# Optimization experiments

Measured on AMD Instinct MI355X. Metric: run time of the kernel, lower is better.

The kernel has to match this reference:

```python
import jax, jax.numpy as jnp
import numpy as np

B, D = 512, 1024
NK, DIMS = 160, 3  # hardcoded in the layer: Dense(160*3), reshape (-1,160,3)


def setup_inputs() -> dict:
    key = jax.random.key(0)
    k1, k2 = jax.random.split(key)
    inputs = jax.random.normal(k1, (B, D), dtype=jnp.float32)
    W = jax.random.normal(k2, (D, NK * DIMS), dtype=jnp.float32) * 0.02
    b = jnp.zeros((NK * DIMS,), dtype=jnp.float32)
    return {"inputs": inputs, "W": W, "b": b}


def reference(inputs, W, b):
    # dense projection: [B, D] @ [D, 480] -> [B, 480]
    x = inputs @ W + b
    act = x.reshape(-1, NK, DIMS)                       # [B, 160, 3]
    # pairwise diffs: [B, 160, 3, 1] - [1, 160, 3, B] -> [B, 160, 3, B]
    diffs = act[:, :, :, None] - jnp.transpose(act, (1, 2, 0))[None]
    abs_diffs = jnp.sum(jnp.abs(diffs), axis=2)         # [B, 160, B]
    minibatch_features = jnp.sum(jnp.exp(-abs_diffs), axis=2)  # [B, 160]
    return jnp.concatenate([inputs, minibatch_features], axis=1)  # [B, D+160]
```

## Files before the change

### kernel.cpp

```cpp
#include <hip/hip_runtime.h>
#include <hip/hip_bf16.h>

#define B_SZ 512
#define D_SZ 1024
#define NK 160
#define NCOL 480
#define OUTW 1184
#define LOG2E 1.44269504088896340736f

typedef __attribute__((ext_vector_type(8))) short bf16x8;
typedef __attribute__((ext_vector_type(4))) float f32x4;

__device__ __forceinline__ unsigned int f32_bf16_rne(float f) {
    unsigned int u = __float_as_uint(f);
    u += 0x7fffu + ((u >> 16) & 1u);
    return u >> 16;
}
__device__ __forceinline__ unsigned int pk2(float x, float y) {
    return f32_bf16_rne(x) | (f32_bf16_rne(y) << 16);
}
__device__ __forceinline__ float bf16u_to_f32(unsigned int h) {
    return __uint_as_float(h << 16);
}

__global__ __launch_bounds__(256) void mbd_gemm_kernel(
    const float* __restrict__ A,
    const float* __restrict__ W,
    const float* __restrict__ bias,
    float* __restrict__ out,
    float* __restrict__ act_t)
{
    __shared__ char lds[32768];
    const int bid = blockIdx.x;
    const int t = threadIdx.x;

    {
        const float4 v = *reinterpret_cast<const float4*>(&A[bid * D_SZ + t * 4]);
        *reinterpret_cast<float4*>(&out[bid * OUTW + t * 4]) = v;
    }
    if (bid >= 480) return;

    const int g = bid >> 3;
    const int bm = (bid & 7) * 2 + (g & 1);
    const int bn = g >> 1;
    const int i0 = bm * 32, c0 = bn * 16;
    const int w = __builtin_amdgcn_readfirstlane(t >> 6);
    const int l = t & 63, lhi = l >> 4, llo = l & 15;

    const int arow = t >> 3, aseg = t & 7;
    const int wcol = t & 15, wkb = t >> 4;
    const int aswz = (arow & 7) << 4;
    const int wswz = (wcol & 7) << 4;
    const float* __restrict__ aptr = A + (size_t)(i0 + arow) * D_SZ + aseg * 16;
    const float* __restrict__ wptr = W + (size_t)wkb * 8 * NCOL + (c0 + wcol);

    f32x4 acc = {0.f, 0.f, 0.f, 0.f};
    float4 ra[4];
    float rw[8];

    auto issue_loads = [&](int k0) {
#pragma unroll
        for (int s = 0; s < 4; ++s)
            ra[s] = *reinterpret_cast<const float4*>(aptr + k0 + s * 4);
#pragma unroll
        for (int j = 0; j < 8; ++j)
            rw[j] = wptr[(size_t)(k0 + j) * NCOL];
    };
    auto write_stage = [&](int buf) {
        char* base = lds + buf * 16384;
        uint4 p0, p1;
        p0.x = pk2(ra[0].x, ra[0].y); p0.y = pk2(ra[0].z, ra[0].w);
        p0.z = pk2(ra[1].x, ra[1].y); p0.w = pk2(ra[1].z, ra[1].w);
        p1.x = pk2(ra[2].x, ra[2].y); p1.y = pk2(ra[2].z, ra[2].w);
        p1.z = pk2(ra[3].x, ra[3].y); p1.w = pk2(ra[3].z, ra[3].w);
        char* arp = base + arow * 256;
        *reinterpret_cast<uint4*>(arp + ((aseg * 32) ^ aswz)) = p0;
        *reinterpret_cast<uint4*>(arp + ((aseg * 32 + 16) ^ aswz)) = p1;
        unsigned int h[8]; float lo[8];
#pragma unroll
        for (int j = 0; j < 8; ++j) {
            h[j] = f32_bf16_rne(rw[j]);
            lo[j] = rw[j] - bf16u_to_f32(h[j]);
        }
        uint4 ph, pl;
        ph.x = h[0] | (h[1] << 16); ph.y = h[2] | (h[3] << 16);
        ph.z = h[4] | (h[5] << 16); ph.w = h[6] | (h[7] << 16);
        pl.x = pk2(lo[0], lo[1]); pl.y = pk2(lo[2], lo[3]);
        pl.z = pk2(lo[4], lo[5]); pl.w = pk2(lo[6], lo[7]);
        const int wo = (wkb * 16) ^ wswz;
        *reinterpret_cast<uint4*>(base + 8192 + wcol * 256 + wo) = ph;
        *reinterpret_cast<uint4*>(base + 12288 + wcol * 256 + wo) = pl;
    };
    auto compute = [&](int buf) {
        const char* base = lds + buf * 16384;
        const char* bsrc = base + ((w >= 2) ? 12288 : 8192);
        const int wrow = (w & 1) * 16;
#pragma unroll
        for (int ks = 0; ks < 4; ++ks) {
            const int koff = (lhi * 16 + ks * 64) ^ ((llo & 7) << 4);
            const bf16x8 af = *reinterpret_cast<const bf16x8*>(base + (wrow + llo) * 256 + koff);
            const bf16x8 bf = *reinterpret_cast<const bf16x8*>(bsrc + llo * 256 + koff);
            acc = __builtin_amdgcn_mfma_f32_16x16x32_bf16(af, bf, acc, 0, 0, 0);
        }
    };

    issue_loads(0);
    write_stage(0);
    __syncthreads();
    for (int ch = 0; ch < 8; ++ch) {
        if (ch < 7) issue_loads((ch + 1) * 128);
        compute(ch & 1);
        if (ch < 7) {
            __syncthreads();
            write_stage((ch + 1) & 1);
            __syncthreads();
        }
    }
    __syncthreads();
    float4* comb = reinterpret_cast<float4*>(lds);
    if (w >= 2) comb[(w - 2) * 64 + l] = make_float4(acc[0], acc[1], acc[2], acc[3]);
    __syncthreads();
    if (w < 2) {
        const float4 lo4 = comb[w * 64 + l];
        const int col = c0 + llo;
        const float bs = bias[col];
        float4 o;
        o.x = (acc[0] + lo4.x + bs) * LOG2E;
        o.y = (acc[1] + lo4.y + bs) * LOG2E;
        o.z = (acc[2] + lo4.z + bs) * LOG2E;
        o.w = (acc[3] + lo4.w + bs) * LOG2E;
        *reinterpret_cast<float4*>(&act_t[(size_t)col * B_SZ + i0 + (w & 1) * 16 + lhi * 4]) = o;
    }
}

__global__ __launch_bounds__(64) void mbd_pairwise_kernel(
    const float* __restrict__ act_t,
    float* __restrict__ out)
{
    __shared__ float4 as4[B_SZ];
    const int bid = blockIdx.x;
    const int klin = (bid & 7) * 320 + (bid >> 3);
    const int k = klin >> 4;
    const int c = klin & 15;
    const int t = threadIdx.x;

    const float* __restrict__ p0 = act_t + (size_t)(3 * k + 0) * B_SZ;
    const float* __restrict__ p1 = act_t + (size_t)(3 * k + 1) * B_SZ;
    const float* __restrict__ p2 = act_t + (size_t)(3 * k + 2) * B_SZ;
#pragma unroll
    for (int s = 0; s < 8; ++s) {
        const int idx = t + s * 64;
        as4[idx] = make_float4(p0[idx], p1[idx], p2[idx], 0.f);
    }
    __syncthreads();

    const int jq = t >> 3;
    const int rg = t & 7;
    const int r0 = c * 32 + rg * 4;
    const float4 a0 = as4[r0 + 0];
    const float4 a1 = as4[r0 + 1];
    const float4 a2 = as4[r0 + 2];
    const float4 a3 = as4[r0 + 3];

    float acc0 = 0.f, acc1 = 0.f, acc2 = 0.f, acc3 = 0.f;
#pragma unroll 8
    for (int jj = 0; jj < 64; ++jj) {
        const float4 av = as4[jq + jj * 8];
        acc0 += __builtin_amdgcn_exp2f(-(fabsf(a0.x - av.x) + fabsf(a0.y - av.y) + fabsf(a0.z - av.z)));
        acc1 += __builtin_amdgcn_exp2f(-(fabsf(a1.x - av.x) + fabsf(a1.y - av.y) + fabsf(a1.z - av.z)));
        acc2 += __builtin_amdgcn_exp2f(-(fabsf(a2.x - av.x) + fabsf(a2.y - av.y) + fabsf(a2.z - av.z)));
        acc3 += __builtin_amdgcn_exp2f(-(fabsf(a3.x - av.x) + fabsf(a3.y - av.y) + fabsf(a3.z - av.z)));
    }
#pragma unroll
    for (int m = 8; m <= 32; m <<= 1) {
        acc0 += __shfl_xor(acc0, m);
        acc1 += __shfl_xor(acc1, m);
        acc2 += __shfl_xor(acc2, m);
        acc3 += __shfl_xor(acc3, m);
    }
    if (t < 8) {
        out[(size_t)(r0 + 0) * OUTW + D_SZ + k] = acc0;
        out[(size_t)(r0 + 1) * OUTW + D_SZ + k] = acc1;
        out[(size_t)(r0 + 2) * OUTW + D_SZ + k] = acc2;
        out[(size_t)(r0 + 3) * OUTW + D_SZ + k] = acc3;
    }
}

extern "C" void kernel_launch(void* const* d_in, const int* in_sizes, int n_in,
                              void* d_out, int out_size, void* d_ws, size_t ws_size,
                              hipStream_t stream)
{
    const float* inputs = (const float*)d_in[0];
    const float* W      = (const float*)d_in[1];
    const float* bias   = (const float*)d_in[2];
    float* out = (float*)d_out;
    float* act_t = (float*)d_ws;

    mbd_gemm_kernel<<<512, 256, 0, stream>>>(inputs, W, bias, out, act_t);
    mbd_pairwise_kernel<<<NK * 16, 64, 0, stream>>>(act_t, out);
}
```

Measured before the change: 26.97 us.

## Pre-split W into transposed bf16 hi/lo buffers and use an LDS-free split-K GEMM

```diff
diff --git a/kernel.cpp b/kernel.cpp
--- a/kernel.cpp
+++ b/kernel.cpp
@@ -23,113 +23,94 @@
     return __uint_as_float(h << 16);
 }
 
+__global__ __launch_bounds__(256) void mbd_prep_kernel(
+    const float* __restrict__ A,
+    const float* __restrict__ W,
+    unsigned int* __restrict__ Whi_u,
+    unsigned int* __restrict__ Wlo_u,
+    float* __restrict__ out)
+{
+    __shared__ float lds_t[64][33];
+    const int b = blockIdx.x, t = threadIdx.x;
+    if (b < 512) {
+        const float4 v = *reinterpret_cast<const float4*>(&A[b * D_SZ + t * 4]);
+        *reinterpret_cast<float4*>(&out[b * OUTW + t * 4]) = v;
+        return;
+    }
+    const int bw = b - 512;
+    const int c0 = (bw % 15) * 32;
+    const int k0 = (bw / 15) * 64;
+#pragma unroll
+    for (int p = 0; p < 8; ++p) {
+        const int k = p * 8 + (t >> 5);
+        lds_t[k][t & 31] = W[(k0 + k) * NCOL + c0 + (t & 31)];
+    }
+    __syncthreads();
+#pragma unroll
+    for (int p = 0; p < 4; ++p) {
+        const int flat = p * 256 + t;
+        const int col = flat >> 5;
+        const int kkp = flat & 31;
+        const float w0 = lds_t[2 * kkp + 0][col];
+        const float w1 = lds_t[2 * kkp + 1][col];
+        const unsigned int h0 = f32_bf16_rne(w0), h1 = f32_bf16_rne(w1);
+        const unsigned int l0 = f32_bf16_rne(w0 - bf16u_to_f32(h0));
+        const unsigned int l1 = f32_bf16_rne(w1 - bf16u_to_f32(h1));
+        const int idx = (c0 + col) * 512 + (k0 >> 1) + kkp;
+        Whi_u[idx] = h0 | (h1 << 16);
+        Wlo_u[idx] = l0 | (l1 << 16);
+    }
+}
+
 __global__ __launch_bounds__(256) void mbd_gemm_kernel(
     const float* __restrict__ A,
-    const float* __restrict__ W,
+    const unsigned int* __restrict__ Whi_u,
+    const unsigned int* __restrict__ Wlo_u,
     const float* __restrict__ bias,
-    float* __restrict__ out,
     float* __restrict__ act_t)
 {
-    __shared__ char lds[32768];
+    __shared__ f32x4 comb[4][64];
     const int bid = blockIdx.x;
+    const int loc = bid >> 3;
+    const int bm = (bid & 7) * 4 + loc / 30;
+    const int bn = loc % 30;
+    const int i0 = bm * 16, c0 = bn * 16;
     const int t = threadIdx.x;
-
-    {
-        const float4 v = *reinterpret_cast<const float4*>(&A[bid * D_SZ + t * 4]);
-        *reinterpret_cast<float4*>(&out[bid * OUTW + t * 4]) = v;
-    }
-    if (bid >= 480) return;
-
-    const int g = bid >> 3;
-    const int bm = (bid & 7) * 2 + (g & 1);
-    const int bn = g >> 1;
-    const int i0 = bm * 32, c0 = bn * 16;
-    const int w = __builtin_amdgcn_readfirstlane(t >> 6);
+    const int kq = t >> 6;
     const int l = t & 63, lhi = l >> 4, llo = l & 15;
 
-    const int arow = t >> 3, aseg = t & 7;
-    const int wcol = t & 15, wkb = t >> 4;
-    const int aswz = (arow & 7) << 4;
-    const int wswz = (wcol & 7) << 4;
-    const float* __restrict__ aptr = A + (size_t)(i0 + arow) * D_SZ + aseg * 16;
-    const float* __restrict__ wptr = W + (size_t)wkb * 8 * NCOL + (c0 + wcol);
+    const float* __restrict__ arow = A + (size_t)(i0 + llo) * D_SZ;
+    const unsigned int* __restrict__ whp = Whi_u + (size_t)(c0 + llo) * 512;
+    const unsigned int* __restrict__ wlp = Wlo_u + (size_t)(c0 + llo) * 512;
 
     f32x4 acc = {0.f, 0.f, 0.f, 0.f};
-    float4 ra[4];
-    float rw[8];
-
-    auto issue_loads = [&](int k0) {
+    const int kb = kq * 256 + lhi * 8;
 #pragma unroll
-        for (int s = 0; s < 4; ++s)
-            ra[s] = *reinterpret_cast<const float4*>(aptr + k0 + s * 4);
-#pragma unroll
-        for (int j = 0; j < 8; ++j)
-            rw[j] = wptr[(size_t)(k0 + j) * NCOL];
-    };
-    auto write_stage = [&](int buf) {
-        char* base = lds + buf * 16384;
-        uint4 p0, p1;
-        p0.x = pk2(ra[0].x, ra[0].y); p0.y = pk2(ra[0].z, ra[0].w);
-        p0.z = pk2(ra[1].x, ra[1].y); p0.w = pk2(ra[1].z, ra[1].w);
-        p1.x = pk2(ra[2].x, ra[2].y); p1.y = pk2(ra[2].z, ra[2].w);
-        p1.z = pk2(ra[3].x, ra[3].y); p1.w = pk2(ra[3].z, ra[3].w);
-        char* arp = base + arow * 256;
-        *reinterpret_cast<uint4*>(arp + ((aseg * 32) ^ aswz)) = p0;
-        *reinterpret_cast<uint4*>(arp + ((aseg * 32 + 16) ^ aswz)) = p1;
-        unsigned int h[8]; float lo[8];
-#pragma unroll
-        for (int j = 0; j < 8; ++j) {
-            h[j] = f32_bf16_rne(rw[j]);
-            lo[j] = rw[j] - bf16u_to_f32(h[j]);
-        }
-        uint4 ph, pl;
-        ph.x = h[0] | (h[1] << 16); ph.y = h[2] | (h[3] << 16);
-        ph.z = h[4] | (h[5] << 16); ph.w = h[6] | (h[7] << 16);
-        pl.x = pk2(lo[0], lo[1]); pl.y = pk2(lo[2], lo[3]);
-        pl.z = pk2(lo[4], lo[5]); pl.w = pk2(lo[6], lo[7]);
-        const int wo = (wkb * 16) ^ wswz;
-        *reinterpret_cast<uint4*>(base + 8192 + wcol * 256 + wo) = ph;
-        *reinterpret_cast<uint4*>(base + 12288 + wcol * 256 + wo) = pl;
-    };
-    auto compute = [&](int buf) {
-        const char* base = lds + buf * 16384;
-        const char* bsrc = base + ((w >= 2) ? 12288 : 8192);
-        const int wrow = (w & 1) * 16;
-#pragma unroll
-        for (int ks = 0; ks < 4; ++ks) {
-            const int koff = (lhi * 16 + ks * 64) ^ ((llo & 7) << 4);
-            const bf16x8 af = *reinterpret_cast<const bf16x8*>(base + (wrow + llo) * 256 + koff);
-            const bf16x8 bf = *reinterpret_cast<const bf16x8*>(bsrc + llo * 256 + koff);
-            acc = __builtin_amdgcn_mfma_f32_16x16x32_bf16(af, bf, acc, 0, 0, 0);
-        }
-    };
-
-    issue_loads(0);
-    write_stage(0);
+    for (int ks = 0; ks < 8; ++ks) {
+        const int k0 = kb + ks * 32;
+        const float4 a0 = *reinterpret_cast<const float4*>(arow + k0);
+        const float4 a1 = *reinterpret_cast<const float4*>(arow + k0 + 4);
+        uint4 ap;
+        ap.x = pk2(a0.x, a0.y); ap.y = pk2(a0.z, a0.w);
+        ap.z = pk2(a1.x, a1.y); ap.w = pk2(a1.z, a1.w);
+        const bf16x8 af = __builtin_bit_cast(bf16x8, ap);
+        const bf16x8 wh = *reinterpret_cast<const bf16x8*>(whp + (k0 >> 1));
+        const bf16x8 wl = *reinterpret_cast<const bf16x8*>(wlp + (k0 >> 1));
+        acc = __builtin_amdgcn_mfma_f32_16x16x32_bf16(af, wh, acc, 0, 0, 0);
+        acc = __builtin_amdgcn_mfma_f32_16x16x32_bf16(af, wl, acc, 0, 0, 0);
+    }
+    comb[kq][l] = acc;
     __syncthreads();
-    for (int ch = 0; ch < 8; ++ch) {
-        if (ch < 7) issue_loads((ch + 1) * 128);
-        compute(ch & 1);
-        if (ch < 7) {
-            __syncthreads();
-            write_stage((ch + 1) & 1);
-            __syncthreads();
-        }
-    }
-    __syncthreads();
-    float4* comb = reinterpret_cast<float4*>(lds);
-    if (w >= 2) comb[(w - 2) * 64 + l] = make_float4(acc[0], acc[1], acc[2], acc[3]);
-    __syncthreads();
-    if (w < 2) {
-        const float4 lo4 = comb[w * 64 + l];
+    if (t < 64) {
+        const f32x4 s = comb[0][l] + comb[1][l] + comb[2][l] + comb[3][l];
         const int col = c0 + llo;
         const float bs = bias[col];
         float4 o;
-        o.x = (acc[0] + lo4.x + bs) * LOG2E;
-        o.y = (acc[1] + lo4.y + bs) * LOG2E;
-        o.z = (acc[2] + lo4.z + bs) * LOG2E;
-        o.w = (acc[3] + lo4.w + bs) * LOG2E;
-        *reinterpret_cast<float4*>(&act_t[(size_t)col * B_SZ + i0 + (w & 1) * 16 + lhi * 4]) = o;
+        o.x = (s[0] + bs) * LOG2E;
+        o.y = (s[1] + bs) * LOG2E;
+        o.z = (s[2] + bs) * LOG2E;
+        o.w = (s[3] + bs) * LOG2E;
+        *reinterpret_cast<float4*>(&act_t[(size_t)col * B_SZ + i0 + lhi * 4]) = o;
     }
 }
 
@@ -194,8 +175,13 @@
     const float* W      = (const float*)d_in[1];
     const float* bias   = (const float*)d_in[2];
     float* out = (float*)d_out;
-    float* act_t = (float*)d_ws;
 
-    mbd_gemm_kernel<<<512, 256, 0, stream>>>(inputs, W, bias, out, act_t);
+    char* ws = (char*)d_ws;
+    unsigned int* Whi_u = (unsigned int*)(ws);
+    unsigned int* Wlo_u = (unsigned int*)(ws + 983040);
+    float*        act_t = (float*)      (ws + 2 * 983040);
+
+    mbd_prep_kernel<<<752, 256, 0, stream>>>(inputs, W, Whi_u, Wlo_u, out);
+    mbd_gemm_kernel<<<960, 256, 0, stream>>>(inputs, Whi_u, Wlo_u, bias, act_t);
     mbd_pairwise_kernel<<<NK * 16, 64, 0, stream>>>(act_t, out);
 }
```

Measured after the change: 39.06 us. 1.45x slower.

## Drop split-bf16 W precision, restructure GEMM K-split, move input copy to pairwise kernel

Applied to the files above, without the earlier changes.

```diff
diff --git a/kernel.cpp b/kernel.cpp
--- a/kernel.cpp
+++ b/kernel.cpp
@@ -19,130 +19,131 @@
 __device__ __forceinline__ unsigned int pk2(float x, float y) {
     return f32_bf16_rne(x) | (f32_bf16_rne(y) << 16);
 }
-__device__ __forceinline__ float bf16u_to_f32(unsigned int h) {
-    return __uint_as_float(h << 16);
-}
 
 __global__ __launch_bounds__(256) void mbd_gemm_kernel(
     const float* __restrict__ A,
     const float* __restrict__ W,
     const float* __restrict__ bias,
-    float* __restrict__ out,
     float* __restrict__ act_t)
 {
-    __shared__ char lds[32768];
+    __shared__ char lds[49152];
     const int bid = blockIdx.x;
+    const int loc = bid >> 3;
+    const int bm = (bid & 7) * 2 + (loc & 1);
+    const int bn = loc >> 1;
+    const int i0 = bm * 32, c0 = bn * 16;
     const int t = threadIdx.x;
-
-    {
-        const float4 v = *reinterpret_cast<const float4*>(&A[bid * D_SZ + t * 4]);
-        *reinterpret_cast<float4*>(&out[bid * OUTW + t * 4]) = v;
-    }
-    if (bid >= 480) return;
-
-    const int g = bid >> 3;
-    const int bm = (bid & 7) * 2 + (g & 1);
-    const int bn = g >> 1;
-    const int i0 = bm * 32, c0 = bn * 16;
     const int w = __builtin_amdgcn_readfirstlane(t >> 6);
     const int l = t & 63, lhi = l >> 4, llo = l & 15;
 
     const int arow = t >> 3, aseg = t & 7;
-    const int wcol = t & 15, wkb = t >> 4;
+    const int wcol = t & 15, wkg = t >> 4;
     const int aswz = (arow & 7) << 4;
     const int wswz = (wcol & 7) << 4;
-    const float* __restrict__ aptr = A + (size_t)(i0 + arow) * D_SZ + aseg * 16;
-    const float* __restrict__ wptr = W + (size_t)wkb * 8 * NCOL + (c0 + wcol);
-
-    f32x4 acc = {0.f, 0.f, 0.f, 0.f};
-    float4 ra[4];
-    float rw[8];
+    const float* __restrict__ aptr = A + (size_t)(i0 + arow) * D_SZ + aseg * 32;
+    const float* __restrict__ wptr = W + (size_t)wkg * 16 * NCOL + c0 + wcol;
+
+    float4 ra[8];
+    float rw[16];
+    f32x4 acc0 = {0.f, 0.f, 0.f, 0.f}, acc1 = {0.f, 0.f, 0.f, 0.f};
 
     auto issue_loads = [&](int k0) {
 #pragma unroll
-        for (int s = 0; s < 4; ++s)
-            ra[s] = *reinterpret_cast<const float4*>(aptr + k0 + s * 4);
-#pragma unroll
-        for (int j = 0; j < 8; ++j)
+        for (int q = 0; q < 8; ++q)
+            ra[q] = *reinterpret_cast<const float4*>(aptr + k0 + q * 4);
+#pragma unroll
+        for (int j = 0; j < 16; ++j)
             rw[j] = wptr[(size_t)(k0 + j) * NCOL];
     };
     auto write_stage = [&](int buf) {
-        char* base = lds + buf * 16384;
+        char* base = lds + buf * 24576;
+        char* arp = base + arow * 512;
+#pragma unroll
+        for (int q = 0; q < 4; ++q) {
+            uint4 p;
+            p.x = pk2(ra[2 * q].x, ra[2 * q].y);
+            p.y = pk2(ra[2 * q].z, ra[2 * q].w);
+            p.z = pk2(ra[2 * q + 1].x, ra[2 * q + 1].y);
+            p.w = pk2(ra[2 * q + 1].z, ra[2 * q + 1].w);
+            *reinterpret_cast<uint4*>(arp + ((aseg * 64 + q * 16) ^ aswz)) = p;
+        }
+        char* wrp = base + 16384 + wcol * 512;
         uint4 p0, p1;
-        p0.x = pk2(ra[0].x, ra[0].y); p0.y = pk2(ra[0].z, ra[0].w);
-        p0.z = pk2(ra[1].x, ra[1].y); p0.w = pk2(ra[1].z, ra[1].w);
-        p1.x = pk2(ra[2].x, ra[2].y); p1.y = pk2(ra[2].z, ra[2].w);
-        p1.z = pk2(ra[3].x, ra[3].y); p1.w = pk2(ra[3].z, ra[3].w);
-        char* arp = base + arow * 256;
-        *reinterpret_cast<uint4*>(arp + ((aseg * 32) ^ aswz)) = p0;
-        *reinterpret_cast<uint4*>(arp + ((aseg * 32 + 16) ^ aswz)) = p1;
-        unsigned int h[8]; float lo[8];
-#pragma unroll
-        for (int j = 0; j < 8; ++j) {
-            h[j] = f32_bf16_rne(rw[j]);
-            lo[j] = rw[j] - bf16u_to_f32(h[j]);
-        }
-        uint4 ph, pl;
-        ph.x = h[0] | (h[1] << 16); ph.y = h[2] | (h[3] << 16);
-        ph.z = h[4] | (h[5] << 16); ph.w = h[6] | (h[7] << 16);
-        pl.x = pk2(lo[0], lo[1]); pl.y = pk2(lo[2], lo[3]);
-        pl.z = pk2(lo[4], lo[5]); pl.w = pk2(lo[6], lo[7]);
-        const int wo = (wkb * 16) ^ wswz;
-        *reinterpret_cast<uint4*>(base + 8192 + wcol * 256 + wo) = ph;
-        *reinterpret_cast<uint4*>(base + 12288 + wcol * 256 + wo) = pl;
+        p0.x = pk2(rw[0], rw[1]);  p0.y = pk2(rw[2], rw[3]);
+        p0.z = pk2(rw[4], rw[5]);  p0.w = pk2(rw[6], rw[7]);
+        p1.x = pk2(rw[8], rw[9]);  p1.y = pk2(rw[10], rw[11]);
+        p1.z = pk2(rw[12], rw[13]); p1.w = pk2(rw[14], rw[15]);
+        *reinterpret_cast<uint4*>(wrp + ((wkg * 32) ^ wswz)) = p0;
+        *reinterpret_cast<uint4*>(wrp + ((wkg * 32 + 16) ^ wswz)) = p1;
     };
     auto compute = [&](int buf) {
-        const char* base = lds + buf * 16384;
-        const char* bsrc = base + ((w >= 2) ? 12288 : 8192);
-        const int wrow = (w & 1) * 16;
-#pragma unroll
-        for (int ks = 0; ks < 4; ++ks) {
-            const int koff = (lhi * 16 + ks * 64) ^ ((llo & 7) << 4);
-            const bf16x8 af = *reinterpret_cast<const bf16x8*>(base + (wrow + llo) * 256 + koff);
-            const bf16x8 bf = *reinterpret_cast<const bf16x8*>(bsrc + llo * 256 + koff);
-            acc = __builtin_amdgcn_mfma_f32_16x16x32_bf16(af, bf, acc, 0, 0, 0);
+        const char* base = lds + buf * 24576;
+        const int rswz = (llo & 7) << 4;
+#pragma unroll
+        for (int ks2 = 0; ks2 < 2; ++ks2) {
+            const int kb = (lhi * 16 + (2 * w + ks2) * 64) ^ rswz;
+            const bf16x8 af0 = *reinterpret_cast<const bf16x8*>(base + llo * 512 + kb);
+            const bf16x8 af1 = *reinterpret_cast<const bf16x8*>(base + (16 + llo) * 512 + kb);
+            const bf16x8 bf  = *reinterpret_cast<const bf16x8*>(base + 16384 + llo * 512 + kb);
+            acc0 = __builtin_amdgcn_mfma_f32_16x16x32_bf16(af0, bf, acc0, 0, 0, 0);
+            acc1 = __builtin_amdgcn_mfma_f32_16x16x32_bf16(af1, bf, acc1, 0, 0, 0);
         }
     };
 
     issue_loads(0);
     write_stage(0);
     __syncthreads();
-    for (int ch = 0; ch < 8; ++ch) {
-        if (ch < 7) issue_loads((ch + 1) * 128);
+    for (int ch = 0; ch < 4; ++ch) {
+        if (ch < 3) issue_loads((ch + 1) * 256);
         compute(ch & 1);
-        if (ch < 7) {
+        if (ch < 3) {
             __syncthreads();
             write_stage((ch + 1) & 1);
             __syncthreads();
         }
     }
     __syncthreads();
-    float4* comb = reinterpret_cast<float4*>(lds);
-    if (w >= 2) comb[(w - 2) * 64 + l] = make_float4(acc[0], acc[1], acc[2], acc[3]);
-    __syncthreads();
-    if (w < 2) {
-        const float4 lo4 = comb[w * 64 + l];
-        const int col = c0 + llo;
+    f32x4* comb = reinterpret_cast<f32x4*>(lds);
+    comb[(w * 2 + 0) * 64 + l] = acc0;
+    comb[(w * 2 + 1) * 64 + l] = acc1;
+    __syncthreads();
+    if (t < 128) {
+        const int th = t >> 6;
+        const int l2 = t & 63, llo2 = l2 & 15, lhi2 = l2 >> 4;
+        f32x4 s = comb[(0 + th) * 64 + l2] + comb[(2 + th) * 64 + l2]
+                + comb[(4 + th) * 64 + l2] + comb[(6 + th) * 64 + l2];
+        const int col = c0 + llo2;
         const float bs = bias[col];
         float4 o;
-        o.x = (acc[0] + lo4.x + bs) * LOG2E;
-        o.y = (acc[1] + lo4.y + bs) * LOG2E;
-        o.z = (acc[2] + lo4.z + bs) * LOG2E;
-        o.w = (acc[3] + lo4.w + bs) * LOG2E;
-        *reinterpret_cast<float4*>(&act_t[(size_t)col * B_SZ + i0 + (w & 1) * 16 + lhi * 4]) = o;
+        o.x = (s[0] + bs) * LOG2E;
+        o.y = (s[1] + bs) * LOG2E;
+        o.z = (s[2] + bs) * LOG2E;
+        o.w = (s[3] + bs) * LOG2E;
+        *reinterpret_cast<float4*>(&act_t[(size_t)col * B_SZ + i0 + th * 16 + lhi2 * 4]) = o;
     }
 }
 
 __global__ __launch_bounds__(64) void mbd_pairwise_kernel(
+    const float* __restrict__ A,
     const float* __restrict__ act_t,
     float* __restrict__ out)
 {
     __shared__ float4 as4[B_SZ];
     const int bid = blockIdx.x;
+    const int t = threadIdx.x;
+
+    if (bid < 512) {
+#pragma unroll
+        for (int s = 0; s < 4; ++s) {
+            const int idx = t + s * 64;
+            const float4 v = *reinterpret_cast<const float4*>(&A[bid * D_SZ + idx * 4]);
+            *reinterpret_cast<float4*>(&out[bid * OUTW + idx * 4]) = v;
+        }
+    }
+
     const int klin = (bid & 7) * 320 + (bid >> 3);
     const int k = klin >> 4;
     const int c = klin & 15;
-    const int t = threadIdx.x;
 
     const float* __restrict__ p0 = act_t + (size_t)(3 * k + 0) * B_SZ;
     const float* __restrict__ p1 = act_t + (size_t)(3 * k + 1) * B_SZ;
@@ -196,6 +197,6 @@
     float* out = (float*)d_out;
     float* act_t = (float*)d_ws;
 
-    mbd_gemm_kernel<<<512, 256, 0, stream>>>(inputs, W, bias, out, act_t);
-    mbd_pairwise_kernel<<<NK * 16, 64, 0, stream>>>(act_t, out);
-}
+    mbd_gemm_kernel<<<480, 256, 0, stream>>>(inputs, W, bias, act_t);
+    mbd_pairwise_kernel<<<NK * 16, 64, 0, stream>>>(inputs, act_t, out);
+}
```

Result: slower. 30.31 us (+12.4%).

## Split-K GEMM with single bf16 W, move input copy into pairwise kernel

Applied to the files above, without the earlier changes.

```diff
diff --git a/kernel.cpp b/kernel.cpp
--- a/kernel.cpp
+++ b/kernel.cpp
@@ -7,6 +7,7 @@
 #define NCOL 480
 #define OUTW 1184
 #define LOG2E 1.44269504088896340736f
+#define PLANE 245760
 
 typedef __attribute__((ext_vector_type(8))) short bf16x8;
 typedef __attribute__((ext_vector_type(4))) float f32x4;
@@ -19,170 +20,164 @@
 __device__ __forceinline__ unsigned int pk2(float x, float y) {
     return f32_bf16_rne(x) | (f32_bf16_rne(y) << 16);
 }
-__device__ __forceinline__ float bf16u_to_f32(unsigned int h) {
-    return __uint_as_float(h << 16);
-}
 
 __global__ __launch_bounds__(256) void mbd_gemm_kernel(
     const float* __restrict__ A,
     const float* __restrict__ W,
     const float* __restrict__ bias,
-    float* __restrict__ out,
-    float* __restrict__ act_t)
+    float* __restrict__ act2)
 {
     __shared__ char lds[32768];
     const int bid = blockIdx.x;
+    const int xcd = bid & 7, loc = bid >> 3;
+    const int bm = xcd * 2 + (loc & 1);
+    const int ksp = (loc >> 1) & 1;
+    const int bn = loc >> 2;
+    const int i0 = bm * 32, c0 = bn * 32, kb0 = ksp * 512;
     const int t = threadIdx.x;
-
-    {
-        const float4 v = *reinterpret_cast<const float4*>(&A[bid * D_SZ + t * 4]);
-        *reinterpret_cast<float4*>(&out[bid * OUTW + t * 4]) = v;
-    }
-    if (bid >= 480) return;
-
-    const int g = bid >> 3;
-    const int bm = (bid & 7) * 2 + (g & 1);
-    const int bn = g >> 1;
-    const int i0 = bm * 32, c0 = bn * 16;
     const int w = __builtin_amdgcn_readfirstlane(t >> 6);
     const int l = t & 63, lhi = l >> 4, llo = l & 15;
 
     const int arow = t >> 3, aseg = t & 7;
-    const int wcol = t & 15, wkb = t >> 4;
+    const int wcol = t & 31, wkg = t >> 5;
     const int aswz = (arow & 7) << 4;
     const int wswz = (wcol & 7) << 4;
-    const float* __restrict__ aptr = A + (size_t)(i0 + arow) * D_SZ + aseg * 16;
-    const float* __restrict__ wptr = W + (size_t)wkb * 8 * NCOL + (c0 + wcol);
+    const float* __restrict__ aptr = A + (size_t)(i0 + arow) * D_SZ + kb0 + aseg * 16;
+    const float* __restrict__ wptr = W + (size_t)(kb0 + wkg * 16) * NCOL + c0 + wcol;
 
+    float4 ra[4];
+    float rw[16];
     f32x4 acc = {0.f, 0.f, 0.f, 0.f};
-    float4 ra[4];
-    float rw[8];
 
     auto issue_loads = [&](int k0) {
 #pragma unroll
         for (int s = 0; s < 4; ++s)
             ra[s] = *reinterpret_cast<const float4*>(aptr + k0 + s * 4);
 #pragma unroll
-        for (int j = 0; j < 8; ++j)
+        for (int j = 0; j < 16; ++j)
             rw[j] = wptr[(size_t)(k0 + j) * NCOL];
     };
     auto write_stage = [&](int buf) {
         char* base = lds + buf * 16384;
+        char* arp = base + arow * 256;
         uint4 p0, p1;
         p0.x = pk2(ra[0].x, ra[0].y); p0.y = pk2(ra[0].z, ra[0].w);
         p0.z = pk2(ra[1].x, ra[1].y); p0.w = pk2(ra[1].z, ra[1].w);
         p1.x = pk2(ra[2].x, ra[2].y); p1.y = pk2(ra[2].z, ra[2].w);
         p1.z = pk2(ra[3].x, ra[3].y); p1.w = pk2(ra[3].z, ra[3].w);
-        char* arp = base + arow * 256;
         *reinterpret_cast<uint4*>(arp + ((aseg * 32) ^ aswz)) = p0;
         *reinterpret_cast<uint4*>(arp + ((aseg * 32 + 16) ^ aswz)) = p1;
-        unsigned int h[8]; float lo[8];
-#pragma unroll
-        for (int j = 0; j < 8; ++j) {
-            h[j] = f32_bf16_rne(rw[j]);
-            lo[j] = rw[j] - bf16u_to_f32(h[j]);
-        }
-        uint4 ph, pl;
-        ph.x = h[0] | (h[1] << 16); ph.y = h[2] | (h[3] << 16);
-        ph.z = h[4] | (h[5] << 16); ph.w = h[6] | (h[7] << 16);
-        pl.x = pk2(lo[0], lo[1]); pl.y = pk2(lo[2], lo[3]);
-        pl.z = pk2(lo[4], lo[5]); pl.w = pk2(lo[6], lo[7]);
-        const int wo = (wkb * 16) ^ wswz;
-        *reinterpret_cast<uint4*>(base + 8192 + wcol * 256 + wo) = ph;
-        *reinterpret_cast<uint4*>(base + 12288 + wcol * 256 + wo) = pl;
+        char* wrp = base + 8192 + wcol * 256;
+        uint4 q0, q1;
+        q0.x = pk2(rw[0], rw[1]);   q0.y = pk2(rw[2], rw[3]);
+        q0.z = pk2(rw[4], rw[5]);   q0.w = pk2(rw[6], rw[7]);
+        q1.x = pk2(rw[8], rw[9]);   q1.y = pk2(rw[10], rw[11]);
+        q1.z = pk2(rw[12], rw[13]); q1.w = pk2(rw[14], rw[15]);
+        *reinterpret_cast<uint4*>(wrp + ((wkg * 32) ^ wswz)) = q0;
+        *reinterpret_cast<uint4*>(wrp + ((wkg * 32 + 16) ^ wswz)) = q1;
     };
     auto compute = [&](int buf) {
         const char* base = lds + buf * 16384;
-        const char* bsrc = base + ((w >= 2) ? 12288 : 8192);
-        const int wrow = (w & 1) * 16;
+        const int r0 = (w & 1) * 16, cc = (w >> 1) * 16;
+        const int lswz = (llo & 7) << 4;
 #pragma unroll
         for (int ks = 0; ks < 4; ++ks) {
-            const int koff = (lhi * 16 + ks * 64) ^ ((llo & 7) << 4);
-            const bf16x8 af = *reinterpret_cast<const bf16x8*>(base + (wrow + llo) * 256 + koff);
-            const bf16x8 bf = *reinterpret_cast<const bf16x8*>(bsrc + llo * 256 + koff);
+            const int koff = (lhi * 16 + ks * 64) ^ lswz;
+            const bf16x8 af = *reinterpret_cast<const bf16x8*>(base + (r0 + llo) * 256 + koff);
+            const bf16x8 bf = *reinterpret_cast<const bf16x8*>(base + 8192 + (cc + llo) * 256 + koff);
             acc = __builtin_amdgcn_mfma_f32_16x16x32_bf16(af, bf, acc, 0, 0, 0);
         }
     };
 
     issue_loads(0);
     write_stage(0);
+    issue_loads(128);
     __syncthreads();
-    for (int ch = 0; ch < 8; ++ch) {
-        if (ch < 7) issue_loads((ch + 1) * 128);
+    for (int ch = 0; ch < 4; ++ch) {
         compute(ch & 1);
-        if (ch < 7) {
-            __syncthreads();
+        if (ch < 3) {
             write_stage((ch + 1) & 1);
+            if (ch < 2) issue_loads((ch + 2) * 128);
             __syncthreads();
         }
     }
-    __syncthreads();
-    float4* comb = reinterpret_cast<float4*>(lds);
-    if (w >= 2) comb[(w - 2) * 64 + l] = make_float4(acc[0], acc[1], acc[2], acc[3]);
-    __syncthreads();
-    if (w < 2) {
-        const float4 lo4 = comb[w * 64 + l];
-        const int col = c0 + llo;
-        const float bs = bias[col];
-        float4 o;
-        o.x = (acc[0] + lo4.x + bs) * LOG2E;
-        o.y = (acc[1] + lo4.y + bs) * LOG2E;
-        o.z = (acc[2] + lo4.z + bs) * LOG2E;
-        o.w = (acc[3] + lo4.w + bs) * LOG2E;
-        *reinterpret_cast<float4*>(&act_t[(size_t)col * B_SZ + i0 + (w & 1) * 16 + lhi * 4]) = o;
-    }
+
+    const int r0 = (w & 1) * 16, cc = (w >> 1) * 16;
+    const int col = c0 + cc + llo;
+    const float bs = ksp ? 0.f : bias[col];
+    float4 o;
+    o.x = (acc[0] + bs) * LOG2E;
+    o.y = (acc[1] + bs) * LOG2E;
+    o.z = (acc[2] + bs) * LOG2E;
+    o.w = (acc[3] + bs) * LOG2E;
+    *reinterpret_cast<float4*>(
+        &act2[(size_t)ksp * PLANE + (size_t)col * B_SZ + i0 + r0 + lhi * 4]) = o;
 }
 
 __global__ __launch_bounds__(64) void mbd_pairwise_kernel(
-    const float* __restrict__ act_t,
+    const float* __restrict__ A,
+    const float* __restrict__ act2,
     float* __restrict__ out)
 {
     __shared__ float4 as4[B_SZ];
     const int bid = blockIdx.x;
-    const int klin = (bid & 7) * 320 + (bid >> 3);
-    const int k = klin >> 4;
-    const int c = klin & 15;
     const int t = threadIdx.x;
 
-    const float* __restrict__ p0 = act_t + (size_t)(3 * k + 0) * B_SZ;
-    const float* __restrict__ p1 = act_t + (size_t)(3 * k + 1) * B_SZ;
-    const float* __restrict__ p2 = act_t + (size_t)(3 * k + 2) * B_SZ;
+    if (bid < 512) {
+#pragma unroll
+        for (int s = 0; s < 4; ++s) {
+            const int idx = t + s * 64;
+            const float4 v = *reinterpret_cast<const float4*>(&A[bid * D_SZ + idx * 4]);
+            *reinterpret_cast<float4*>(&out[bid * OUTW + idx * 4]) = v;
+        }
+    }
+
+    const int klin = (bid & 7) * 160 + (bid >> 3);
+    const int k = klin >> 3;
+    const int c = klin & 7;
+
+    const float* __restrict__ p0 = act2 + (size_t)(3 * k + 0) * B_SZ;
+    const float* __restrict__ p1 = act2 + (size_t)(3 * k + 1) * B_SZ;
+    const float* __restrict__ p2 = act2 + (size_t)(3 * k + 2) * B_SZ;
 #pragma unroll
     for (int s = 0; s < 8; ++s) {
         const int idx = t + s * 64;
-        as4[idx] = make_float4(p0[idx], p1[idx], p2[idx], 0.f);
+        as4[idx] = make_float4(p0[idx] + p0[idx + PLANE],
+                               p1[idx] + p1[idx + PLANE],
+                               p2[idx] + p2[idx + PLANE], 0.f);
     }
     __syncthreads();
 
     const int jq = t >> 3;
     const int rg = t & 7;
-    const int r0 = c * 32 + rg * 4;
-    const float4 a0 = as4[r0 + 0];
-    const float4 a1 = as4[r0 + 1];
-    const float4 a2 = as4[r0 + 2];
-    const float4 a3 = as4[r0 + 3];
+    const int r0 = c * 64 + rg * 8;
+    float ax[8], ay[8], az[8];
+#pragma unroll
+    for (int i = 0; i < 8; ++i) {
+        const float4 v = as4[r0 + i];
+        ax[i] = v.x; ay[i] = v.y; az[i] = v.z;
+    }
+    float acc[8];
+#pragma unroll
+    for (int i = 0; i < 8; ++i) acc[i] = 0.f;
 
-    float acc0 = 0.f, acc1 = 0.f, acc2 = 0.f, acc3 = 0.f;
-#pragma unroll 8
+#pragma unroll 4
     for (int jj = 0; jj < 64; ++jj) {
         const float4 av = as4[jq + jj * 8];
-        acc0 += __builtin_amdgcn_exp2f(-(fabsf(a0.x - av.x) + fabsf(a0.y - av.y) + fabsf(a0.z - av.z)));
-        acc1 += __builtin_amdgcn_exp2f(-(fabsf(a1.x - av.x) + fabsf(a1.y - av.y) + fabsf(a1.z - av.z)));
-        acc2 += __builtin_amdgcn_exp2f(-(fabsf(a2.x - av.x) + fabsf(a2.y - av.y) + fabsf(a2.z - av.z)));
-        acc3 += __builtin_amdgcn_exp2f(-(fabsf(a3.x - av.x) + fabsf(a3.y - av.y) + fabsf(a3.z - av.z)));
+#pragma unroll
+        for (int i = 0; i < 8; ++i)
+            acc[i] += __builtin_amdgcn_exp2f(
+                -(fabsf(ax[i] - av.x) + fabsf(ay[i] - av.y) + fabsf(az[i] - av.z)));
     }
 #pragma unroll
     for (int m = 8; m <= 32; m <<= 1) {
-        acc0 += __shfl_xor(acc0, m);
-        acc1 += __shfl_xor(acc1, m);
-        acc2 += __shfl_xor(acc2, m);
-        acc3 += __shfl_xor(acc3, m);
+#pragma unroll
+        for (int i = 0; i < 8; ++i) acc[i] += __shfl_xor(acc[i], m);
     }
     if (t < 8) {
-        out[(size_t)(r0 + 0) * OUTW + D_SZ + k] = acc0;
-        out[(size_t)(r0 + 1) * OUTW + D_SZ + k] = acc1;
-        out[(size_t)(r0 + 2) * OUTW + D_SZ + k] = acc2;
-        out[(size_t)(r0 + 3) * OUTW + D_SZ + k] = acc3;
+#pragma unroll
+        for (int i = 0; i < 8; ++i)
+            out[(size_t)(r0 + i) * OUTW + D_SZ + k] = acc[i];
     }
 }
 
@@ -194,8 +189,8 @@
     const float* W      = (const float*)d_in[1];
     const float* bias   = (const float*)d_in[2];
     float* out = (float*)d_out;
-    float* act_t = (float*)d_ws;
+    float* act2 = (float*)d_ws;
 
-    mbd_gemm_kernel<<<512, 256, 0, stream>>>(inputs, W, bias, out, act_t);
-    mbd_pairwise_kernel<<<NK * 16, 64, 0, stream>>>(act_t, out);
+    mbd_gemm_kernel<<<480, 256, 0, stream>>>(inputs, W, bias, act2);
+    mbd_pairwise_kernel<<<1280, 64, 0, stream>>>(inputs, act2, out);
 }
```

Result: slower. 27.78 us (+3.0%).
